# Optimization experiments

Measured on AMD Instinct MI355X. Metric: run time of the kernel, lower is better.

Reference implementation:

```python
import jax, jax.numpy as jnp
import numpy as np

IMAGE_W, IMAGE_H = 1024, 800
STRIDES = (8, 16, 32, 64, 128)
LEVEL_HW = ((100, 128), (50, 64), (25, 32), (13, 16), (7, 8))
TOP_N = 1000
MIN_SCORE = 0.01
NMS_THR = 0.6
MAX_DET = 100
NUM_CLASSES = 80
BATCH = 16


def _grid(h, w, stride, b):
    ys = (jnp.arange(h, dtype=jnp.float32) + 0.5) * stride
    xs = (jnp.arange(w, dtype=jnp.float32) + 0.5) * stride
    gx, gy = jnp.meshgrid(xs, ys)  # [h, w]
    pos = jnp.stack([gx, gy], axis=-1)  # [h, w, 2] = (x, y)
    return jnp.broadcast_to(pos, (b, h, w, 2))


def setup_inputs() -> dict:
    key = jax.random.key(0)
    inp = {}
    for i, ((h, w), s) in enumerate(zip(LEVEL_HW, STRIDES)):
        key, k1, k2, k3 = jax.random.split(key, 4)
        inp[f"cls{i}"] = jax.random.normal(k1, (BATCH, h, w, NUM_CLASSES), jnp.float32)
        # +3 so exp(reg) gives realistic ~20px box extents
        inp[f"reg{i}"] = jax.random.normal(k2, (BATCH, h, w, 4), jnp.float32) + 3.0
        inp[f"ctr{i}"] = jax.random.normal(k3, (BATCH, h, w, 1), jnp.float32)
        inp[f"pos{i}"] = _grid(h, w, s, BATCH)
    return inp


def _level_filter(cls, reg, ctr, pos):
    b = cls.shape[0]
    cls = jax.nn.sigmoid(cls).reshape(b, -1, NUM_CLASSES)
    reg = jnp.exp(reg).reshape(b, -1, 4)
    ctr = jax.nn.sigmoid(ctr).reshape(b, -1)
    pos = pos.reshape(b, -1, 2)
    scores = jnp.sqrt(jnp.max(cls, axis=2) * ctr)  # [b, n]
    classes = jnp.argmax(cls, axis=2)  # [b, n] int
    if scores.shape[1] >= TOP_N:
        scores, idx = jax.lax.top_k(scores, TOP_N)
        classes = jnp.take_along_axis(classes, idx, axis=1)
        reg = jnp.take_along_axis(reg, idx[..., None], axis=1)
        pos = jnp.take_along_axis(pos, idx[..., None], axis=1)
        cls = jnp.take_along_axis(cls, idx[..., None], axis=1)
    return scores, classes, reg, pos, cls


def _decode_boxes(reg, pos):
    # ltrb offsets -> x1y1x2y2, truncate to int (torch .int()), clamp to image
    xy_min = pos - reg[..., 0:2]
    xy_max = pos + reg[..., 2:4]
    bx = jnp.trunc(jnp.concatenate([xy_min, xy_max], axis=-1))
    x1 = jnp.maximum(bx[..., 0], 0.0)
    y1 = jnp.maximum(bx[..., 1], 0.0)
    x2 = jnp.minimum(bx[..., 2], IMAGE_W - 1.0)
    y2 = jnp.minimum(bx[..., 3], IMAGE_H - 1.0)
    return jnp.stack([x1, y1, x2, y2], axis=-1)


def _nms_image(scores, classes, boxes, clsp):
    valid = scores > MIN_SCORE
    order = jnp.argsort(jnp.where(valid, -scores, jnp.inf))  # valid, desc score first
    s = scores[order]
    c = classes[order].astype(jnp.float32)
    b = boxes[order]
    cp = clsp[order]
    v = valid[order]
    # pairwise IoU (keep/suppress decisions are not differentiated)
    bb = jax.lax.stop_gradient(b)
    area = (bb[:, 2] - bb[:, 0]) * (bb[:, 3] - bb[:, 1])
    lt = jnp.maximum(bb[:, None, :2], bb[None, :, :2])
    rb = jnp.minimum(bb[:, None, 2:], bb[None, :, 2:])
    wh = jnp.maximum(rb - lt, 0.0)
    inter = wh[..., 0] * wh[..., 1]
    iou = inter / (area[:, None] + area[None, :] - inter)
    n = s.shape[0]
    idxs = jnp.arange(n)

    def body(i, keep):
        sup = keep[i] & (iou[i] > NMS_THR) & (idxs > i)
        return keep & ~sup

    keep = jax.lax.fori_loop(0, n, body, v)
    rank = jnp.cumsum(keep) - 1
    slot = jnp.where(keep & (rank < MAX_DET), rank, MAX_DET)  # MAX_DET -> dropped
    out_s = jnp.full((MAX_DET,), -1.0, jnp.float32).at[slot].set(s, mode="drop")
    out_c = jnp.full((MAX_DET,), -1.0, jnp.float32).at[slot].set(c, mode="drop")
    out_b = jnp.full((MAX_DET, 4), -1.0, jnp.float32).at[slot].set(b, mode="drop")
    out_cp = jnp.full((MAX_DET, NUM_CLASSES), -1.0, jnp.float32).at[slot].set(cp, mode="drop")
    return out_s, out_c, out_b, out_cp


def reference(cls0, cls1, cls2, cls3, cls4, reg0, reg1, reg2, reg3, reg4,
              ctr0, ctr1, ctr2, ctr3, ctr4, pos0, pos1, pos2, pos3, pos4):
    clss = [cls0, cls1, cls2, cls3, cls4]
    regs = [reg0, reg1, reg2, reg3, reg4]
    ctrs = [ctr0, ctr1, ctr2, ctr3, ctr4]
    poss = [pos0, pos1, pos2, pos3, pos4]
    parts = [_level_filter(c, r, t, p) for c, r, t, p in zip(clss, regs, ctrs, poss)]
    scores = jnp.concatenate([p[0] for p in parts], axis=1)
    classes = jnp.concatenate([p[1] for p in parts], axis=1)
    reg = jnp.concatenate([p[2] for p in parts], axis=1)
    pos = jnp.concatenate([p[3] for p in parts], axis=1)
    clsp = jnp.concatenate([p[4] for p in parts], axis=1)
    boxes = _decode_boxes(reg, pos)
    return jax.vmap(_nms_image)(scores, classes, boxes, clsp)
```

## Files before the change

### kernel.cpp

```cpp
#include <hip/hip_runtime.h>
#include <math.h>

#define TOTAL_G 17064
#define BATCHN  16
#define ALLF    0xFFFFFFFFFFFFFFFFull
#define INVALID_HI 0xC3DC28F5u

typedef unsigned long long u64;
typedef unsigned int u32;
typedef unsigned short u16;

#define KEYS0_OFF   0
#define KEYS1_OFF   1638400
#define KEYS234_OFF 2048000
#define CLSI_OFF    2187264
#define NC_OFF      2733312
#define T01_OFF     2733568
#define T512_OFF    2733824
#define KR_OFF      2733952
#define MSK_OFF     2799488
#define SLOTK_OFF   3323776

struct Ptrs {
  const float *cls0,*cls1,*cls2,*cls3,*cls4;
  const float *reg0,*reg1,*reg2,*reg3,*reg4;
  const float *ctr0,*ctr1,*ctr2,*ctr3,*ctr4;
  const float *pos0,*pos1,*pos2,*pos3,*pos4;
  char *ws;
};

__device__ __forceinline__ float sigd(float x) {
  return (float)(1.0 / (1.0 + exp(-(double)x)));
}
__device__ __forceinline__ float dexp(float x) {
  return (float)exp((double)x);
}
__device__ __forceinline__ void levinfo(int gid, int& lev, int& idx, int& nl) {
  if      (gid < 12800) { lev=0; idx=gid;        nl=12800; }
  else if (gid < 16000) { lev=1; idx=gid-12800;  nl=3200;  }
  else if (gid < 16800) { lev=2; idx=gid-16000;  nl=800;   }
  else if (gid < 17008) { lev=3; idx=gid-16800;  nl=208;   }
  else                  { lev=4; idx=gid-17008;  nl=56;    }
}

__device__ __forceinline__ u64* krank_of(char* ws, int b) {
  return (u64*)(ws + KR_OFF + (size_t)b * 4096);
}
__device__ __forceinline__ u64* msk_of(char* ws, int b) {
  return (u64*)(ws + MSK_OFF + (size_t)b * 32768);
}
__device__ __forceinline__ u64* slotkey_of(char* ws, int b) {
  return (u64*)(ws + SLOTK_OFF + (size_t)b * 800);
}

__device__ __forceinline__ float4 decode_box(const Ptrs& P, int b, int gid) {
  int lev, idx, nl; levinfo(gid, lev, idx, nl);
  const float *rp, *pp;
  if      (lev == 0) { rp = P.reg0; pp = P.pos0; }
  else if (lev == 1) { rp = P.reg1; pp = P.pos1; }
  else if (lev == 2) { rp = P.reg2; pp = P.pos2; }
  else if (lev == 3) { rp = P.reg3; pp = P.pos3; }
  else               { rp = P.reg4; pp = P.pos4; }
  float4 rv = *(const float4*)(rp + (size_t)(b * nl + idx) * 4);
  float2 pv = *(const float2*)(pp + (size_t)(b * nl + idx) * 2);
  float e0 = dexp(rv.x), e1 = dexp(rv.y), e2 = dexp(rv.z), e3 = dexp(rv.w);
  float x1 = truncf(pv.x - e0), y1 = truncf(pv.y - e1);
  float x2 = truncf(pv.x + e2), y2 = truncf(pv.y + e3);
  x1 = fmaxf(x1, 0.0f); y1 = fmaxf(y1, 0.0f);
  x2 = fminf(x2, 1023.0f); y2 = fminf(y2, 799.0f);
  return make_float4(x1, y1, x2, y2);
}

__global__ __launch_bounds__(256) void k_score(Ptrs P) {
  __shared__ float4 sk4[64 * 20];
  int b = blockIdx.y;
  int tid = threadIdx.x;
  int p0 = blockIdx.x * 64;

  #pragma unroll
  for (int it = 0; it < 5; ++it) {
    int t4 = it * 256 + tid;
    int g = p0 + t4 / 20;
    if (g < TOTAL_G) {
      int sub = t4 - (t4 / 20) * 20;
      int lev, idx, nl; levinfo(g, lev, idx, nl);
      const float* clsb;
      if      (lev == 0) clsb = P.cls0;
      else if (lev == 1) clsb = P.cls1;
      else if (lev == 2) clsb = P.cls2;
      else if (lev == 3) clsb = P.cls3;
      else               clsb = P.cls4;
      sk4[t4] = ((const float4*)(clsb + (size_t)(b * nl + idx) * 80))[sub];
    }
  }
  __syncthreads();

  int lp = tid >> 2, q = tid & 3;
  int g = p0 + lp;
  if (g >= TOTAL_G) return;

  const float4* my4 = &sk4[lp * 20 + q * 5];
  float m = -INFINITY, m2 = -INFINITY; int mi = 0;
  #pragma unroll
  for (int k = 0; k < 5; ++k) {
    float4 v = my4[k];
    int base = q * 20 + 4 * k;
    if (v.x > m) { m2 = m; m = v.x; mi = base+0; } else if (v.x > m2) m2 = v.x;
    if (v.y > m) { m2 = m; m = v.y; mi = base+1; } else if (v.y > m2) m2 = v.y;
    if (v.z > m) { m2 = m; m = v.z; mi = base+2; } else if (v.z > m2) m2 = v.z;
    if (v.w > m) { m2 = m; m = v.w; mi = base+3; } else if (v.w > m2) m2 = v.w;
  }
  #pragma unroll
  for (int xw = 1; xw <= 2; xw <<= 1) {
    float om  = __shfl_xor(m,  xw);
    float om2 = __shfl_xor(m2, xw);
    int   omi = __shfl_xor(mi, xw);
    bool take = (om > m) || (om == m && omi < mi);
    float lm  = take ? m : om;
    float wm2 = take ? om2 : m2;
    if (take) { m = om; mi = omi; }
    m2 = fmaxf(lm, wm2);
  }

  float thr = fminf(m - 1e-3f, 9.0f);
  float pmax; int ci;
  if (m2 >= thr) {
    float pv = -1.0f; int pi = 0x7fffffff;
    #pragma unroll 1
    for (int k = 0; k < 5; ++k) {
      float4 v = my4[k];
      float xs[4] = {v.x, v.y, v.z, v.w};
      #pragma unroll
      for (int e = 0; e < 4; ++e) {
        if (xs[e] >= thr) {
          float p = sigd(xs[e]);
          if (p > pv) { pv = p; pi = q * 20 + 4 * k + e; }
        }
      }
    }
    #pragma unroll
    for (int xw = 1; xw <= 2; xw <<= 1) {
      float ov = __shfl_xor(pv, xw);
      int   oi = __shfl_xor(pi, xw);
      if (ov > pv || (ov == pv && oi < pi)) { pv = ov; pi = oi; }
    }
    pmax = pv; ci = pi;
  } else {
    pmax = sigd(m); ci = mi;
  }

  if (q == 0) {
    int lev, idx, nl; levinfo(g, lev, idx, nl);
    const float* ctrb;
    if      (lev == 0) ctrb = P.ctr0;
    else if (lev == 1) ctrb = P.ctr1;
    else if (lev == 2) ctrb = P.ctr2;
    else if (lev == 3) ctrb = P.ctr3;
    else               ctrb = P.ctr4;
    float tc = ctrb[(size_t)b * nl + idx];
    float csig = sigd(tc);
    float prod = pmax * csig;
    float s = (float)sqrt((double)prod);
    ((u16*)(P.ws + CLSI_OFF))[(size_t)b * TOTAL_G + g] = (u16)ci;
    unsigned hi = ~__float_as_uint(s);
    u64 key = ((u64)hi << 15) | (unsigned)g;
    if      (lev == 0) ((u64*)(P.ws + KEYS0_OFF))  [(size_t)b * 12800 + idx] = key;
    else if (lev == 1) ((u64*)(P.ws + KEYS1_OFF))  [(size_t)b * 3200  + idx] = key;
    else               ((u64*)(P.ws + KEYS234_OFF))[(size_t)b * 1088  + (g - 16000)] = key;
  }
}

struct SelSh {
  u32 hist[4][4096];
  u64 buf[64];
  u64 res, pfx;
  int t, mode, cnt;
};

__device__ __forceinline__ u64 loadkey(const Ptrs& P, int b, int u) {
  if (u < 12800) return ((const u64*)(P.ws + KEYS0_OFF))  [(size_t)b * 12800 + u];
  if (u < 16000) return ((const u64*)(P.ws + KEYS1_OFF))  [(size_t)b * 3200  + (u - 12800)];
  return               ((const u64*)(P.ws + KEYS234_OFF))[(size_t)b * 1088  + (u - 16000)];
}
__device__ __forceinline__ bool keep_pred(u64 k, int u, u64 T0, u64 T1) {
  bool valid = (u32)(k >> 15) < INVALID_HI;
  bool sel = (u < 12800) ? (k <= T0) : ((u < 16000) ? (k <= T1) : true);
  return valid && sel;
}

__device__ u64 fast_select(const Ptrs& P, int b, const u64* keys, int n,
                           int pred, int t0, SelSh* S) {
  int tid = threadIdx.x, wid = tid >> 6, lane = tid & 63;
  int rep = wid & 3;
  u64 Pfx = 3; int t = t0;
  const int SS[4] = {33, 21, 9, 0};
  const int WW[4] = {12, 12, 12, 9};
  #pragma unroll 1
  for (int p = 0; p < 4; ++p) {
    int s = SS[p], wb = WW[p];
    u32 dmask = (1u << wb) - 1u;
    for (int i = tid; i < 4 * 4096; i += 1024) (&S->hist[0][0])[i] = 0;
    if (tid == 0) { S->mode = 0; S->cnt = 0; }
    __syncthreads();
    int N = pred ? TOTAL_G : n;
    for (int i = tid; i < N; i += 1024) {
      u64 k = pred ? loadkey(P, b, i) : keys[i];
      if (pred == 2 && !((u32)(k >> 15) < INVALID_HI)) continue;
      if ((k >> (s + wb)) == Pfx)
        atomicAdd(&S->hist[rep][(u32)(k >> s) & dmask], 1u);
    }
    __syncthreads();
    for (int i = tid; i < 4096; i += 1024) {
      u32 v = S->hist[0][i] + S->hist[1][i] + S->hist[2][i] + S->hist[3][i];
      S->hist[0][i] = v;
    }
    __syncthreads();
    if (wid == 0) {
      u32 ssum = 0;
      #pragma unroll 8
      for (int i = 0; i < 64; ++i) {
        int ii = (i + lane) & 63;
        ssum += S->hist[0][(lane << 6) + ii];
      }
      u32 inc = ssum;
      for (int o = 1; o < 64; o <<= 1) { u32 v = __shfl_up(inc, o); if (lane >= o) inc += v; }
      u64 ball = __ballot(inc >= (u32)t);
      if (!ball) {
        if (lane == 0) { S->mode = 9; S->res = ALLF; }
      } else {
        int Wq = __ffsll(ball) - 1;
        u32 cumBefore = __shfl(inc - ssum, Wq);
        u32 v2 = S->hist[0][(Wq << 6) + lane];
        u32 inc2 = v2;
        for (int o = 1; o < 64; o <<= 1) { u32 x = __shfl_up(inc2, o); if (lane >= o) inc2 += x; }
        u64 ball2 = __ballot(cumBefore + inc2 >= (u32)t);
        int l2 = __ffsll(ball2) - 1;
        u32 cumB2 = __shfl(cumBefore + inc2 - v2, l2);
        u32 c = __shfl(v2, l2);
        if (lane == 0) {
          int d = (Wq << 6) + l2;
          u64 np = (Pfx << wb) | (u32)d;
          S->pfx = np; S->t = t - (int)cumB2;
          if (s == 0)       { S->mode = 9; S->res = np; }
          else if (c == 1)  { S->mode = 1; }
          else if (c <= 64) { S->mode = 2; }
        }
      }
    }
    __syncthreads();
    int mode = S->mode; u64 np = S->pfx; int tt = S->t;
    if (mode == 9) return S->res;
    if (mode == 1 || mode == 2) {
      int N2 = pred ? TOTAL_G : n;
      for (int i = tid; i < N2; i += 1024) {
        u64 k = pred ? loadkey(P, b, i) : keys[i];
        if (pred == 2 && !((u32)(k >> 15) < INVALID_HI)) continue;
        if ((k >> s) == np) {
          if (mode == 1) S->res = k;
          else { int pos = atomicAdd(&S->cnt, 1); S->buf[pos] = k; }
        }
      }
      __syncthreads();
      if (mode == 2 && wid == 0) {
        int c2 = S->cnt;
        u64 kl = (lane < c2) ? S->buf[lane] : ALLF;
        int r = 0;
        for (int j = 0; j < c2; ++j) r += (S->buf[j] < kl) ? 1 : 0;
        if (lane < c2 && r == tt - 1) S->res = kl;
      }
      __syncthreads();
      return S->res;
    }
    Pfx = np; t = tt;
    __syncthreads();
  }
  return S->pfx;
}

__global__ __launch_bounds__(1024) void k_sel(Ptrs P) {
  __shared__ SelSh S;
  int b = blockIdx.x, which = blockIdx.y;
  u64 T;
  if (which == 0)
    T = fast_select(P, b, (const u64*)(P.ws + KEYS0_OFF) + (size_t)b * 12800, 12800, 0, 1000, &S);
  else if (which == 1)
    T = fast_select(P, b, (const u64*)(P.ws + KEYS1_OFF) + (size_t)b * 3200, 3200, 0, 1000, &S);
  else
    T = fast_select(P, b, (const u64*)0, 0, 2, 512, &S);
  if (threadIdx.x == 0) {
    if      (which == 0) ((u64*)(P.ws + T01_OFF))[b] = T;
    else if (which == 1) ((u64*)(P.ws + T01_OFF))[16 + b] = T;
    else                 ((u64*)(P.ws + T512_OFF))[b] = T;
  }
}

__global__ __launch_bounds__(1024) void k_mask(Ptrs P) {
  __shared__ u64 skey[512];
  __shared__ float4 sbox[512];
  __shared__ u16 srank[512];
  __shared__ u16 parts[1024];
  __shared__ u64 smaskR[512 * 8];
  __shared__ int wbase[272];
  __shared__ int sN5;
  int qi = blockIdx.x, b = blockIdx.y;
  int tid = threadIdx.x, wid = tid >> 6, lane = tid & 63;
  char* ws = P.ws;
  u64 T512 = ((u64*)(ws + T512_OFF))[b];

  for (int it = 0; it < 17; ++it) {
    int u = it * 1024 + tid;
    bool keep5 = false;
    if (u < TOTAL_G) {
      u64 k = loadkey(P, b, u);
      keep5 = ((u32)(k >> 15) < INVALID_HI) && (k <= T512);
    }
    u64 bal = __ballot(keep5);
    if (lane == 0) wbase[it * 16 + wid] = __popcll(bal);
  }
  for (int i = tid; i < 512 * 8; i += 1024) smaskR[i] = 0ull;
  __syncthreads();
  if (wid == 0) {
    int carry = 0;
    for (int base = 0; base < 272; base += 64) {
      int idx = base + lane;
      int v = (idx < 272) ? wbase[idx] : 0;
      int inc = v;
      for (int o = 1; o < 64; o <<= 1) { int x = __shfl_up(inc, o); if (lane >= o) inc += x; }
      if (idx < 272) wbase[idx] = inc - v + carry;
      carry += __shfl(inc, 63);
    }
    if (lane == 0) sN5 = carry;
  }
  __syncthreads();
  int n512 = sN5;
  if (qi == 0 && tid == 0) ((int*)(ws + NC_OFF))[16 + b] = n512;

  for (int it = 0; it < 17; ++it) {
    int u = it * 1024 + tid;
    bool keep5 = false; u64 k = 0;
    if (u < TOTAL_G) {
      k = loadkey(P, b, u);
      keep5 = ((u32)(k >> 15) < INVALID_HI) && (k <= T512);
    }
    u64 bal = __ballot(keep5);
    int pos = wbase[it * 16 + wid] + __popcll(bal & ((1ull << lane) - 1ull));
    if (keep5) skey[pos] = k;
  }
  __syncthreads();
  if (tid < 512) {
    if (tid < n512) {
      sbox[tid] = decode_box(P, b, (int)(skey[tid] & 0x7FFF));
    } else {
      skey[tid] = (ALLF - 511) + (u64)tid;
      sbox[tid] = make_float4(-1e30f, -1e30f, -1e30f, -1e30f);
    }
  }
  __syncthreads();

  {
    int t2 = tid & 511, half = tid >> 9;
    u64 mykey = skey[t2];
    int jb = half << 8, cnt = 0;
    #pragma unroll 4
    for (int j = jb; j < jb + 256; ++j) cnt += (skey[j] < mykey) ? 1 : 0;
    parts[tid] = (u16)cnt;
  }
  __syncthreads();
  if (tid < 512) srank[tid] = (u16)(parts[tid] + parts[tid + 512]);
  __syncthreads();

  int i = qi * 128 + (tid >> 3);
  int w = tid & 7;
  float4 bi = sbox[i];
  u64 ki = skey[i];
  int ri = srank[i];
  float ia = (bi.z - bi.x) * (bi.w - bi.y);
  #pragma unroll 8
  for (int bj = 0; bj < 64; ++bj) {
    int jj = (bj + w) & 63;
    int j = (w << 6) | jj;
    u64 kj = skey[j];
    if (ki < kj) {
      float4 bj4 = sbox[j];
      float ja  = (bj4.z - bj4.x) * (bj4.w - bj4.y);
      float ltx = fmaxf(bi.x, bj4.x), lty = fmaxf(bi.y, bj4.y);
      float rbx = fminf(bi.z, bj4.z), rby = fminf(bi.w, bj4.w);
      float wv = fmaxf(rbx - ltx, 0.0f), hv = fmaxf(rby - lty, 0.0f);
      float inter = wv * hv;
      float iou = inter / (ia + ja - inter);
      if (iou > 0.6f) {
        int rj = srank[j];
        atomicOr(&smaskR[ri * 8 + (rj >> 6)], 1ull << (rj & 63));
      }
    }
  }
  __syncthreads();

  {
    int il = tid >> 3, ww = tid & 7;
    int ig = qi * 128 + il;
    if (ig < n512) {
      int r = srank[ig];
      msk_of(ws, b)[r * 8 + ww] = smaskR[r * 8 + ww];
      if (ww == 0) krank_of(ws, b)[r] = skey[ig];
    }
  }
}

__global__ __launch_bounds__(256) void k_reduce(Ptrs P) {
  __shared__ u64 smask[4096];
  __shared__ u32 keeplist[100];
  __shared__ int keptS;
  __shared__ u64 liveC[267];
  __shared__ u64 pk[256];
  __shared__ int pc[256];
  __shared__ float4 fkb[100];
  __shared__ u64 bk; __shared__ int bc2;

  int b = blockIdx.x;
  int tid = threadIdx.x;
  char* ws = P.ws;
  int n512 = ((int*)(ws + NC_OFF))[16 + b];
  const u64* kr = krank_of(ws, b);

  const u64* gmask = msk_of(ws, b);
  for (int t = tid; t < 4096; t += 256) smask[t] = gmask[t];
  __syncthreads();

  if (tid < 64) {
    int lane = tid;
    u64 lw = 0;
    if (lane < 8) {
      int lo = lane << 6;
      int c = n512 - lo; if (c < 0) c = 0; if (c > 64) c = 64;
      lw = (c >= 64) ? ALLF : ((c > 0) ? ((1ull << c) - 1ull) : 0ull);
    }
    int kept = 0;
    while (kept < 100) {
      bool nz = (lane < 8) && (lw != 0ull);
      u64 bal = __ballot(nz);
      if (!bal) break;
      int W = __ffsll(bal) - 1;
      u64 wv = __shfl(lw, W);
      int bit = __ffsll(wv) - 1;
      int i = (W << 6) + bit;
      if (lane == 0) keeplist[kept] = (u32)i;
      kept++;
      if (lane == W) lw &= ~(1ull << bit);
      if (kept == 100) break;
      if (lane < 8) lw &= ~smask[i * 8 + lane];
    }
    if (lane == 0) keptS = kept;
  }
  __syncthreads();
  int kept = keptS;
  int keptW = kept;

  if (kept < 100 && n512 == 512) {
    u64 T0   = ((u64*)(ws + T01_OFF))[b];
    u64 T1   = ((u64*)(ws + T01_OFF))[16 + b];
    u64 T512 = ((u64*)(ws + T512_OFF))[b];
    for (int w = tid; w < 267; w += 256) {
      int lo = w << 6;
      u64 m = 0;
      for (int e = 0; e < 64; ++e) {
        int u = lo + e;
        if (u < TOTAL_G) {
          u64 k = loadkey(P, b, u);
          if (keep_pred(k, u, T0, T1) && k > T512) m |= (1ull << e);
        }
      }
      liveC[w] = m;
    }
    if (tid < kept) fkb[tid] = decode_box(P, b, (int)(kr[keeplist[tid]] & 0x7FFF));
    __syncthreads();

    for (int k2 = 0; k2 < kept; ++k2) {
      float4 bi = fkb[k2];
      float ia = (bi.z - bi.x) * (bi.w - bi.y);
      for (int u = tid; u < TOTAL_G; u += 256) {
        if (!((liveC[u >> 6] >> (u & 63)) & 1ull)) continue;
        float4 bj4 = decode_box(P, b, u);
        float ja  = (bj4.z - bj4.x) * (bj4.w - bj4.y);
        float ltx = fmaxf(bi.x, bj4.x), lty = fmaxf(bi.y, bj4.y);
        float rbx = fminf(bi.z, bj4.z), rby = fminf(bi.w, bj4.w);
        float wv = fmaxf(rbx - ltx, 0.0f), hv = fmaxf(rby - lty, 0.0f);
        float inter = wv * hv;
        float iou = inter / (ia + ja - inter);
        if (iou > 0.6f) atomicAnd(&liveC[u >> 6], ~(1ull << (u & 63)));
      }
    }
    __syncthreads();

    while (kept < 100) {
      u64 mymin = ALLF; int myc = -1;
      for (int u = tid; u < TOTAL_G; u += 256) {
        if (!((liveC[u >> 6] >> (u & 63)) & 1ull)) continue;
        u64 k = loadkey(P, b, u);
        if (k < mymin) { mymin = k; myc = u; }
      }
      pk[tid] = mymin; pc[tid] = myc;
      __syncthreads();
      if (tid < 64) {
        u64 m = pk[tid]; int c0 = pc[tid];
        #pragma unroll
        for (int o = 64; o < 256; o += 64)
          if (pk[tid + o] < m) { m = pk[tid + o]; c0 = pc[tid + o]; }
        for (int o = 32; o > 0; o >>= 1) {
          u64 om = __shfl_down(m, o); int oc = __shfl_down(c0, o);
          if (om < m) { m = om; c0 = oc; }
        }
        if (tid == 0) { bk = m; bc2 = c0; }
      }
      __syncthreads();
      if (bk == ALLF) break;
      int cs = bc2;
      if (tid == 0) {
        slotkey_of(ws, b)[kept] = bk;
        atomicAnd(&liveC[cs >> 6], ~(1ull << (cs & 63)));
      }
      __syncthreads();
      kept++;
      if (kept == 100) break;
      float4 bi = decode_box(P, b, cs);
      float ia = (bi.z - bi.x) * (bi.w - bi.y);
      for (int u = tid; u < TOTAL_G; u += 256) {
        if (!((liveC[u >> 6] >> (u & 63)) & 1ull)) continue;
        float4 bj4 = decode_box(P, b, u);
        float ja  = (bj4.z - bj4.x) * (bj4.w - bj4.y);
        float ltx = fmaxf(bi.x, bj4.x), lty = fmaxf(bi.y, bj4.y);
        float rbx = fminf(bi.z, bj4.z), rby = fminf(bi.w, bj4.w);
        float wv = fmaxf(rbx - ltx, 0.0f), hv = fmaxf(rby - lty, 0.0f);
        float inter = wv * hv;
        float iou = inter / (ia + ja - inter);
        if (iou > 0.6f) atomicAnd(&liveC[u >> 6], ~(1ull << (u & 63)));
      }
      __syncthreads();
    }
  }

  if (tid < 100) {
    if (tid < keptW)     slotkey_of(ws, b)[tid] = kr[keeplist[tid]];
    else if (tid >= kept) slotkey_of(ws, b)[tid] = ALLF;
  }
}

__global__ __launch_bounds__(256) void k_out(Ptrs P, float* out) {
  int b = blockIdx.x, part = blockIdx.y;
  int s0 = part * 10;
  int tid = threadIdx.x;
  const u64* skl = slotkey_of(P.ws, b);

  if (tid < 10) {
    int s = s0 + tid;
    u64 key = skl[s];
    float os = -1.0f, oc = -1.0f;
    float4 bx = make_float4(-1.0f, -1.0f, -1.0f, -1.0f);
    if (key != ALLF) {
      int gid = (int)(key & 0x7FFF);
      os = __uint_as_float(~(u32)(key >> 15));
      oc = (float)((u16*)(P.ws + CLSI_OFF))[(size_t)b * TOTAL_G + gid];
      bx = decode_box(P, b, gid);
    }
    out[b * 100 + s] = os;
    out[1600 + b * 100 + s] = oc;
    *(float4*)(out + 3200 + (size_t)(b * 100 + s) * 4) = bx;
  }

  for (int t = tid; t < 800; t += 256) {
    int sl = t / 80, k = t - sl * 80;
    int s = s0 + sl;
    u64 key = skl[s];
    float val = -1.0f;
    if (key != ALLF) {
      int gid = (int)(key & 0x7FFF);
      int lev, idx, nl; levinfo(gid, lev, idx, nl);
      const float* cp;
      if      (lev == 0) cp = P.cls0;
      else if (lev == 1) cp = P.cls1;
      else if (lev == 2) cp = P.cls2;
      else if (lev == 3) cp = P.cls3;
      else               cp = P.cls4;
      val = sigd(cp[(size_t)(b * nl + idx) * 80 + k]);
    }
    out[9600 + (size_t)(b * 100 + s) * 80 + k] = val;
  }
}

extern "C" void kernel_launch(void* const* d_in, const int* in_sizes, int n_in,
                              void* d_out, int out_size, void* d_ws, size_t ws_size,
                              hipStream_t stream) {
  (void)in_sizes; (void)n_in; (void)out_size; (void)ws_size;
  Ptrs P;
  P.cls0 = (const float*)d_in[0];  P.reg0 = (const float*)d_in[1];
  P.ctr0 = (const float*)d_in[2];  P.pos0 = (const float*)d_in[3];
  P.cls1 = (const float*)d_in[4];  P.reg1 = (const float*)d_in[5];
  P.ctr1 = (const float*)d_in[6];  P.pos1 = (const float*)d_in[7];
  P.cls2 = (const float*)d_in[8];  P.reg2 = (const float*)d_in[9];
  P.ctr2 = (const float*)d_in[10]; P.pos2 = (const float*)d_in[11];
  P.cls3 = (const float*)d_in[12]; P.reg3 = (const float*)d_in[13];
  P.ctr3 = (const float*)d_in[14]; P.pos3 = (const float*)d_in[15];
  P.cls4 = (const float*)d_in[16]; P.reg4 = (const float*)d_in[17];
  P.ctr4 = (const float*)d_in[18]; P.pos4 = (const float*)d_in[19];
  P.ws = (char*)d_ws;

  k_score<<<dim3(267, 16), 256, 0, stream>>>(P);
  k_sel<<<dim3(16, 3), 1024, 0, stream>>>(P);
  k_mask<<<dim3(4, 16), 1024, 0, stream>>>(P);
  k_reduce<<<16, 256, 0, stream>>>(P);
  k_out<<<dim3(16, 10), 256, 0, stream>>>(P, (float*)d_out);
}
```

Measured before the change: 111.6 us.

## Fuse top-512 selection into mask kernel and defer per-level thresholds to reduce

Removes the separate k_sel launch. The global top-512 threshold is now computed redundantly by each of the 4 k_mask blocks per image, using a shared-memory union to fit the selection histograms. The per-level top-1000 thresholds are computed lazily inside k_reduce, only on the fallback path where fewer than 100 boxes survive. This saves a launch and a dependency gap, but makes k_mask repeat the selection 4 times per image and adds serial latency on the rare fallback path.

```diff
diff --git a/kernel.cpp b/kernel.cpp
--- a/kernel.cpp
+++ b/kernel.cpp
@@ -15,7 +15,6 @@
 #define KEYS234_OFF 2048000
 #define CLSI_OFF    2187264
 #define NC_OFF      2733312
-#define T01_OFF     2733568
 #define T512_OFF    2733824
 #define KR_OFF      2733952
 #define MSK_OFF     2799488
@@ -188,8 +187,7 @@
   return valid && sel;
 }
 
-__device__ u64 fast_select(const Ptrs& P, int b, const u64* keys, int n,
-                           int pred, int t0, SelSh* S) {
+__device__ u64 fast_select(const Ptrs& P, int b, int pred, int t0, SelSh* S) {
   int tid = threadIdx.x, wid = tid >> 6, lane = tid & 63;
   int rep = wid & 3;
   u64 Pfx = 3; int t = t0;
@@ -202,9 +200,8 @@
     for (int i = tid; i < 4 * 4096; i += 1024) (&S->hist[0][0])[i] = 0;
     if (tid == 0) { S->mode = 0; S->cnt = 0; }
     __syncthreads();
-    int N = pred ? TOTAL_G : n;
-    for (int i = tid; i < N; i += 1024) {
-      u64 k = pred ? loadkey(P, b, i) : keys[i];
+    for (int i = tid; i < TOTAL_G; i += 1024) {
+      u64 k = loadkey(P, b, i);
       if (pred == 2 && !((u32)(k >> 15) < INVALID_HI)) continue;
       if ((k >> (s + wb)) == Pfx)
         atomicAdd(&S->hist[rep][(u32)(k >> s) & dmask], 1u);
@@ -251,9 +248,8 @@
     int mode = S->mode; u64 np = S->pfx; int tt = S->t;
     if (mode == 9) return S->res;
     if (mode == 1 || mode == 2) {
-      int N2 = pred ? TOTAL_G : n;
-      for (int i = tid; i < N2; i += 1024) {
-        u64 k = pred ? loadkey(P, b, i) : keys[i];
+      for (int i = tid; i < TOTAL_G; i += 1024) {
+        u64 k = loadkey(P, b, i);
         if (pred == 2 && !((u32)(k >> 15) < INVALID_HI)) continue;
         if ((k >> s) == np) {
           if (mode == 1) S->res = k;
@@ -277,35 +273,21 @@
   return S->pfx;
 }
 
-__global__ __launch_bounds__(1024) void k_sel(Ptrs P) {
-  __shared__ SelSh S;
-  int b = blockIdx.x, which = blockIdx.y;
-  u64 T;
-  if (which == 0)
-    T = fast_select(P, b, (const u64*)(P.ws + KEYS0_OFF) + (size_t)b * 12800, 12800, 0, 1000, &S);
-  else if (which == 1)
-    T = fast_select(P, b, (const u64*)(P.ws + KEYS1_OFF) + (size_t)b * 3200, 3200, 0, 1000, &S);
-  else
-    T = fast_select(P, b, (const u64*)0, 0, 2, 512, &S);
-  if (threadIdx.x == 0) {
-    if      (which == 0) ((u64*)(P.ws + T01_OFF))[b] = T;
-    else if (which == 1) ((u64*)(P.ws + T01_OFF))[16 + b] = T;
-    else                 ((u64*)(P.ws + T512_OFF))[b] = T;
-  }
-}
-
 __global__ __launch_bounds__(1024) void k_mask(Ptrs P) {
+  __shared__ union USh {
+    SelSh S;
+    struct { float4 sbox[512]; u64 smaskR[4096]; u16 parts[1024]; } M;
+  } U;
   __shared__ u64 skey[512];
-  __shared__ float4 sbox[512];
   __shared__ u16 srank[512];
-  __shared__ u16 parts[1024];
-  __shared__ u64 smaskR[512 * 8];
   __shared__ int wbase[272];
   __shared__ int sN5;
   int qi = blockIdx.x, b = blockIdx.y;
   int tid = threadIdx.x, wid = tid >> 6, lane = tid & 63;
   char* ws = P.ws;
-  u64 T512 = ((u64*)(ws + T512_OFF))[b];
+
+  u64 T512 = fast_select(P, b, 2, 512, &U.S);
+  if (qi == 0 && tid == 0) ((u64*)(ws + T512_OFF))[b] = T512;
 
   for (int it = 0; it < 17; ++it) {
     int u = it * 1024 + tid;
@@ -317,7 +299,6 @@
     u64 bal = __ballot(keep5);
     if (lane == 0) wbase[it * 16 + wid] = __popcll(bal);
   }
-  for (int i = tid; i < 512 * 8; i += 1024) smaskR[i] = 0ull;
   __syncthreads();
   if (wid == 0) {
     int carry = 0;
@@ -347,14 +328,16 @@
     if (keep5) skey[pos] = k;
   }
   __syncthreads();
+
   if (tid < 512) {
     if (tid < n512) {
-      sbox[tid] = decode_box(P, b, (int)(skey[tid] & 0x7FFF));
+      U.M.sbox[tid] = decode_box(P, b, (int)(skey[tid] & 0x7FFF));
     } else {
       skey[tid] = (ALLF - 511) + (u64)tid;
-      sbox[tid] = make_float4(-1e30f, -1e30f, -1e30f, -1e30f);
-    }
-  }
+      U.M.sbox[tid] = make_float4(-1e30f, -1e30f, -1e30f, -1e30f);
+    }
+  }
+  for (int i = tid; i < 512 * 8; i += 1024) U.M.smaskR[i] = 0ull;
   __syncthreads();
 
   {
@@ -363,15 +346,15 @@
     int jb = half << 8, cnt = 0;
     #pragma unroll 4
     for (int j = jb; j < jb + 256; ++j) cnt += (skey[j] < mykey) ? 1 : 0;
-    parts[tid] = (u16)cnt;
-  }
-  __syncthreads();
-  if (tid < 512) srank[tid] = (u16)(parts[tid] + parts[tid + 512]);
+    U.M.parts[tid] = (u16)cnt;
+  }
+  __syncthreads();
+  if (tid < 512) srank[tid] = (u16)(U.M.parts[tid] + U.M.parts[tid + 512]);
   __syncthreads();
 
   int i = qi * 128 + (tid >> 3);
   int w = tid & 7;
-  float4 bi = sbox[i];
+  float4 bi = U.M.sbox[i];
   u64 ki = skey[i];
   int ri = srank[i];
   float ia = (bi.z - bi.x) * (bi.w - bi.y);
@@ -381,7 +364,7 @@
     int j = (w << 6) | jj;
     u64 kj = skey[j];
     if (ki < kj) {
-      float4 bj4 = sbox[j];
+      float4 bj4 = U.M.sbox[j];
       float ja  = (bj4.z - bj4.x) * (bj4.w - bj4.y);
       float ltx = fmaxf(bi.x, bj4.x), lty = fmaxf(bi.y, bj4.y);
       float rbx = fminf(bi.z, bj4.z), rby = fminf(bi.w, bj4.w);
@@ -390,7 +373,7 @@
       float iou = inter / (ia + ja - inter);
       if (iou > 0.6f) {
         int rj = srank[j];
-        atomicOr(&smaskR[ri * 8 + (rj >> 6)], 1ull << (rj & 63));
+        atomicOr(&U.M.smaskR[ri * 8 + (rj >> 6)], 1ull << (rj & 63));
       }
     }
   }
@@ -401,10 +384,48 @@
     int ig = qi * 128 + il;
     if (ig < n512) {
       int r = srank[ig];
-      msk_of(ws, b)[r * 8 + ww] = smaskR[r * 8 + ww];
+      msk_of(ws, b)[r * 8 + ww] = U.M.smaskR[r * 8 + ww];
       if (ww == 0) krank_of(ws, b)[r] = skey[ig];
     }
   }
+}
+
+__device__ u64 select256(const u64* keys, int n, int t0, u32* hist, u64* shP, int* shT) {
+  u64 Pfx = 3; int t = t0;
+  const int SS[4] = {33, 21, 9, 0};
+  const int WW[4] = {12, 12, 12, 9};
+  for (int p = 0; p < 4; ++p) {
+    int s = SS[p], wb = WW[p];
+    u32 dmask = (1u << wb) - 1u;
+    for (int i = threadIdx.x; i < 4096; i += 256) hist[i] = 0;
+    __syncthreads();
+    for (int i = threadIdx.x; i < n; i += 256) {
+      u64 k = keys[i];
+      if ((k >> (s + wb)) == Pfx) atomicAdd(&hist[(u32)(k >> s) & dmask], 1u);
+    }
+    __syncthreads();
+    if (threadIdx.x < 64) {
+      int lane = threadIdx.x;
+      u32 ssum = 0;
+      for (int i = 0; i < 64; ++i) ssum += hist[(lane << 6) + ((i + lane) & 63)];
+      u32 inc = ssum;
+      for (int o = 1; o < 64; o <<= 1) { u32 v = __shfl_up(inc, o); if (lane >= o) inc += v; }
+      u64 ball = __ballot(inc >= (u32)t);
+      int Wq = __ffsll(ball) - 1;
+      u32 cumBefore = __shfl(inc - ssum, Wq);
+      u32 v2 = hist[(Wq << 6) + lane];
+      u32 inc2 = v2;
+      for (int o = 1; o < 64; o <<= 1) { u32 x = __shfl_up(inc2, o); if (lane >= o) inc2 += x; }
+      u64 ball2 = __ballot(cumBefore + inc2 >= (u32)t);
+      int l2 = __ffsll(ball2) - 1;
+      u32 cumB2 = __shfl(cumBefore + inc2 - v2, l2);
+      if (lane == 0) { *shP = (Pfx << wb) | (u32)((Wq << 6) + l2); *shT = t - (int)cumB2; }
+    }
+    __syncthreads();
+    Pfx = *shP; t = *shT;
+    __syncthreads();
+  }
+  return Pfx;
 }
 
 __global__ __launch_bounds__(256) void k_reduce(Ptrs P) {
@@ -412,9 +433,11 @@
   __shared__ u32 keeplist[100];
   __shared__ int keptS;
   __shared__ u64 liveC[267];
-  __shared__ u64 pk[256];
-  __shared__ int pc[256];
-  __shared__ float4 fkb[100];
+  __shared__ union UF {
+    u32 hist[4096];
+    struct { u64 pk[256]; int pc[256]; float4 fkb[100]; } F;
+  } UF_;
+  __shared__ u64 shP; __shared__ int shT;
   __shared__ u64 bk; __shared__ int bc2;
 
   int b = blockIdx.x;
@@ -457,8 +480,10 @@
   int keptW = kept;
 
   if (kept < 100 && n512 == 512) {
-    u64 T0   = ((u64*)(ws + T01_OFF))[b];
-    u64 T1   = ((u64*)(ws + T01_OFF))[16 + b];
+    u64 T0 = select256((const u64*)(ws + KEYS0_OFF) + (size_t)b * 12800, 12800, 1000,
+                       UF_.hist, &shP, &shT);
+    u64 T1 = select256((const u64*)(ws + KEYS1_OFF) + (size_t)b * 3200, 3200, 1000,
+                       UF_.hist, &shP, &shT);
     u64 T512 = ((u64*)(ws + T512_OFF))[b];
     for (int w = tid; w < 267; w += 256) {
       int lo = w << 6;
@@ -472,11 +497,11 @@
       }
       liveC[w] = m;
     }
-    if (tid < kept) fkb[tid] = decode_box(P, b, (int)(kr[keeplist[tid]] & 0x7FFF));
+    if (tid < kept) UF_.F.fkb[tid] = decode_box(P, b, (int)(kr[keeplist[tid]] & 0x7FFF));
     __syncthreads();
 
     for (int k2 = 0; k2 < kept; ++k2) {
-      float4 bi = fkb[k2];
+      float4 bi = UF_.F.fkb[k2];
       float ia = (bi.z - bi.x) * (bi.w - bi.y);
       for (int u = tid; u < TOTAL_G; u += 256) {
         if (!((liveC[u >> 6] >> (u & 63)) & 1ull)) continue;
@@ -499,13 +524,13 @@
         u64 k = loadkey(P, b, u);
         if (k < mymin) { mymin = k; myc = u; }
       }
-      pk[tid] = mymin; pc[tid] = myc;
+      UF_.F.pk[tid] = mymin; UF_.F.pc[tid] = myc;
       __syncthreads();
       if (tid < 64) {
-        u64 m = pk[tid]; int c0 = pc[tid];
+        u64 m = UF_.F.pk[tid]; int c0 = UF_.F.pc[tid];
         #pragma unroll
         for (int o = 64; o < 256; o += 64)
-          if (pk[tid + o] < m) { m = pk[tid + o]; c0 = pc[tid + o]; }
+          if (UF_.F.pk[tid + o] < m) { m = UF_.F.pk[tid + o]; c0 = UF_.F.pc[tid + o]; }
         for (int o = 32; o > 0; o >>= 1) {
           u64 om = __shfl_down(m, o); int oc = __shfl_down(c0, o);
           if (om < m) { m = om; c0 = oc; }
@@ -540,7 +565,7 @@
   }
 
   if (tid < 100) {
-    if (tid < keptW)     slotkey_of(ws, b)[tid] = kr[keeplist[tid]];
+    if (tid < keptW)      slotkey_of(ws, b)[tid] = kr[keeplist[tid]];
     else if (tid >= kept) slotkey_of(ws, b)[tid] = ALLF;
   }
 }
@@ -605,7 +630,6 @@
   P.ws = (char*)d_ws;
 
   k_score<<<dim3(267, 16), 256, 0, stream>>>(P);
-  k_sel<<<dim3(16, 3), 1024, 0, stream>>>(P);
   k_mask<<<dim3(4, 16), 1024, 0, stream>>>(P);
   k_reduce<<<16, 256, 0, stream>>>(P);
   k_out<<<dim3(16, 10), 256, 0, stream>>>(P, (float*)d_out);
```

Result: faster. 109.3 us (-2.1%).
